# Kernel tuning notes

Hardware: AMD Instinct MI355X
Metric: run time of the kernel (lower is better)

The kernel has to match this reference:

```python
import jax, jax.numpy as jnp
import numpy as np
import math

B, S, E, H = 2, 2048, 1024, 16
D = E // H  # d_head = 64

def setup_inputs() -> dict:
    key = jax.random.key(0)
    ks = jax.random.split(key, 7)
    query = jax.random.normal(ks[0], (B, S, E), dtype=jnp.float32)
    k_in = jax.random.normal(ks[1], (B, S, E), dtype=jnp.float32)
    v_in = jax.random.normal(ks[2], (B, S, E), dtype=jnp.float32)
    # causal mask, broadcastable over batch and heads; mask==0 positions are blocked
    mask = jnp.tril(jnp.ones((S, S), dtype=jnp.int32))[None, None]
    scale = 1.0 / math.sqrt(E)
    w_q = jax.random.normal(ks[3], (E, E), dtype=jnp.float32) * scale
    w_k = jax.random.normal(ks[4], (E, E), dtype=jnp.float32) * scale
    w_v = jax.random.normal(ks[5], (E, E), dtype=jnp.float32) * scale
    w_o = jax.random.normal(ks[6], (E, E), dtype=jnp.float32) * scale
    return {"query": query, "key": k_in, "value": v_in, "mask": mask,
            "w_q": w_q, "w_k": w_k, "w_v": w_v, "w_o": w_o}

def reference(query, key, value, mask, w_q, w_k, w_v, w_o):
    # projections (nn.Linear with no bias: x @ W^T); split heads -> [B,H,S,D]
    q = (query @ w_q.T).reshape(B, S, H, D).transpose(0, 2, 1, 3)
    k = (key @ w_k.T).reshape(B, S, H, D).transpose(0, 2, 1, 3)
    v = (value @ w_v.T).reshape(B, S, H, D).transpose(0, 2, 1, 3)
    # scaled dot-product scores [B,H,S,S]
    scores = jnp.einsum('bhqd,bhkd->bhqk', q, k) / math.sqrt(D)
    scores = jnp.where(mask == 0, jnp.float32(-1e9), scores)
    attn = jax.nn.softmax(scores, axis=-1)  # dropout p=0.0 -> identity
    out = jnp.einsum('bhqk,bhkd->bhqd', attn, v)  # [B,H,S,D]
    out = out.transpose(0, 2, 1, 3).reshape(B, S, E)
    return out @ w_o.T
```

## Files before the change

### kernel.cpp

```cpp
#include <hip/hip_runtime.h>
#include <hip/hip_bf16.h>

#define B_ 2
#define S_ 2048
#define E_ 1024
#define H_ 16
#define D_ 64

typedef __attribute__((ext_vector_type(8))) short bf16x8;
typedef __attribute__((ext_vector_type(4))) float f32x4;

static __device__ __forceinline__ unsigned short f2bf(float x) {
    union { float f; unsigned u; } v; v.f = x;
    unsigned r = v.u + 0x7FFF + ((v.u >> 16) & 1);
    return (unsigned short)(r >> 16);
}

static __device__ __forceinline__ unsigned pack2bf(float a, float b) {
    union { float f; unsigned u; } x, y; x.f = a; y.f = b;
    unsigned ra = x.u + 0x7FFF + ((x.u >> 16) & 1);
    unsigned rb = y.u + 0x7FFF + ((y.u >> 16) & 1);
    return (ra >> 16) | (rb & 0xFFFF0000u);
}

static __device__ __forceinline__ unsigned packtrunc(float a, float b) {
    union { float f; unsigned u; } x, y; x.f = a; y.f = b;
    return __builtin_amdgcn_perm(y.u, x.u, 0x07060302);
}

static __device__ __forceinline__ void async_copy16(const void* gsrc, void* ldst) {
    __builtin_amdgcn_global_load_lds(
        (const __attribute__((address_space(1))) void*)gsrc,
        (__attribute__((address_space(3))) void*)ldst, 16, 0, 0);
}

__global__ void cvt_multi(const float* __restrict__ s0, const float* __restrict__ s1,
                          const float* __restrict__ s2, const float* __restrict__ s3,
                          unsigned short* __restrict__ dst, int n4,
                          float c0, float c1, float c2, float c3) {
    const float* src = (blockIdx.y == 0) ? s0 : (blockIdx.y == 1) ? s1
                     : (blockIdx.y == 2) ? s2 : s3;
    float c = (blockIdx.y == 0) ? c0 : (blockIdx.y == 1) ? c1
            : (blockIdx.y == 2) ? c2 : c3;
    int i = blockIdx.x * blockDim.x + threadIdx.x;
    if (i >= n4) return;
    float4 f = ((const float4*)src)[i];
    ushort4 o;
    o.x = f2bf(f.x * c); o.y = f2bf(f.y * c); o.z = f2bf(f.z * c); o.w = f2bf(f.w * c);
    ((ushort4*)(dst + (size_t)blockIdx.y * n4 * 4))[i] = o;
}

template <int MODE>
__global__ __launch_bounds__(256) void gemm128(
    const unsigned short* __restrict__ A0, const unsigned short* __restrict__ B0,
    void* __restrict__ C0, int M, int N, int K) {
    __shared__ __align__(16) unsigned short Al[128 * 64];
    __shared__ __align__(16) unsigned short Bl[128 * 64];
    const unsigned short* A = A0;
    const unsigned short* Bm = B0;
    int z = 0;
    if (MODE == 4) {
        z = blockIdx.z;
        A  = A0 + (size_t)z * 4194304;
        Bm = B0 + (size_t)z * 1048576;
    }
    const int bm = blockIdx.y * 128, bn = blockIdx.x * 128;
    const int tid = threadIdx.x;
    const int w = tid >> 6, lane = tid & 63;
    const int col = lane & 15, quad = lane >> 4, swz = col & 7;
    const int wm = (w >> 1) * 64, wn = (w & 1) * 64;

    f32x4 acc[4][4] = {};

    for (int k0 = 0; k0 < K; k0 += 64) {
        __syncthreads();
#pragma unroll
        for (int it = 0; it < 4; it++) {
            int s = tid + it * 256, r = s >> 3, cg = (s & 7) ^ (r & 7);
            async_copy16(A + (size_t)(bm + r) * K + k0 + cg * 8, &Al[s * 8]);
            async_copy16(Bm + (size_t)(bn + r) * K + k0 + cg * 8, &Bl[s * 8]);
        }
        __syncthreads();
#pragma unroll
        for (int h = 0; h < 2; h++) {
            const int cq = ((h * 4 + quad) ^ swz) * 8;
            bf16x8 af[4], bf[4];
#pragma unroll
            for (int i = 0; i < 4; i++) af[i] = *(const bf16x8*)&Al[(wm + i * 16 + col) * 64 + cq];
#pragma unroll
            for (int j = 0; j < 4; j++) bf[j] = *(const bf16x8*)&Bl[(wn + j * 16 + col) * 64 + cq];
#pragma unroll
            for (int i = 0; i < 4; i++)
#pragma unroll
                for (int j = 0; j < 4; j++)
                    acc[i][j] = __builtin_amdgcn_mfma_f32_16x16x32_bf16(af[i], bf[j], acc[i][j], 0, 0, 0);
        }
    }

    if (MODE == 3) {
#pragma unroll
        for (int i = 0; i < 4; i++)
#pragma unroll
            for (int j = 0; j < 4; j++)
#pragma unroll
                for (int r = 0; r < 4; r++) {
                    int gm = bm + wm + i * 16 + quad * 4 + r;
                    int gn = bn + wn + j * 16 + col;
                    ((float*)C0)[(size_t)gm * N + gn] = acc[i][j][r];
                }
    } else {
        __syncthreads();
        unsigned short* scr = ((w < 2) ? Al : Bl) + (w & 1) * 4096;
        const int b  = (bm + wm) >> 11;
        const int s0 = (bm + wm) & 2047;
        const int hh = (bn + wn) >> 6;
        unsigned short* outp = (unsigned short*)C0 + (size_t)z * 4194304;
        if (z == 2) {
#pragma unroll
            for (int i = 0; i < 4; i++)
#pragma unroll
                for (int j = 0; j < 4; j++) {
                    int n = j * 16 + col;
                    int c = i * 2 + (quad >> 1);
                    uint2 pk;
                    pk.x = pack2bf(acc[i][j][0], acc[i][j][1]);
                    pk.y = pack2bf(acc[i][j][2], acc[i][j][3]);
                    *(uint2*)&scr[n * 64 + ((c ^ (n & 7)) << 3) + ((quad & 1) << 2)] = pk;
                }
#pragma unroll
            for (int it = 0; it < 8; it++) {
                int slot = it * 64 + lane, n = slot >> 3, c = slot & 7;
                uint4 v = *(uint4*)&scr[n * 64 + ((c ^ (n & 7)) << 3)];
                *(uint4*)&outp[(((size_t)b * H_ + hh) * D_ + n) * S_ + s0 + c * 8] = v;
            }
        } else {
#pragma unroll
            for (int i = 0; i < 4; i++)
#pragma unroll
                for (int j = 0; j < 4; j++)
#pragma unroll
                    for (int r = 0; r < 4; r++) {
                        int m = i * 16 + quad * 4 + r, n = j * 16 + col;
                        scr[m * 64 + (((n >> 3) ^ (m & 7)) << 3) + (n & 7)] = f2bf(acc[i][j][r]);
                    }
#pragma unroll
            for (int it = 0; it < 8; it++) {
                int slot = it * 64 + lane, m = slot >> 3, c = slot & 7;
                uint4 v = *(uint4*)&scr[m * 64 + ((c ^ (m & 7)) << 3)];
                *(uint4*)&outp[(((size_t)b * H_ + hh) * S_ + s0 + m) * (size_t)D_ + c * 8] = v;
            }
        }
    }
}

__global__ __launch_bounds__(256) void attn_kernel(
    const unsigned short* __restrict__ Q, const unsigned short* __restrict__ K_,
    const unsigned short* __restrict__ Vt, unsigned short* __restrict__ Out) {
    __shared__ __align__(16) unsigned short Kl[2][64 * 64];
    __shared__ __align__(16) unsigned short Vl[2][64 * 64];
    const int bh = blockIdx.y;
    const int qb = (bh >= 16) ? (int)blockIdx.x : 15 - (int)blockIdx.x;
    const int q0 = qb * 128;
    const int tid = threadIdx.x;
    const int w = tid >> 6, lane = tid & 63;
    const int col = lane & 15, quad = lane >> 4, swz = col & 7;
    const int qw0 = q0 + w * 32;
    const float NINF = -__builtin_huge_valf();

    const unsigned short* Qh = Q + (size_t)bh * S_ * D_;
    const unsigned short* Kh = K_ + (size_t)bh * S_ * D_;
    const unsigned short* Vh = Vt + (size_t)bh * D_ * S_;

    bf16x8 qf[2][2];
#pragma unroll
    for (int i = 0; i < 2; i++)
#pragma unroll
        for (int h = 0; h < 2; h++)
            qf[i][h] = *(const bf16x8*)(Qh + (size_t)(qw0 + i * 16 + col) * 64 + h * 32 + quad * 8);

    f32x4 o[2][4] = {};
    float lsum[2] = {0.f, 0.f};

#pragma unroll
    for (int it = 0; it < 2; it++) {
        int s = tid + it * 256, r = s >> 3, cg = (s & 7) ^ (r & 7);
        async_copy16(Kh + (size_t)r * 64 + cg * 8, &Kl[0][s * 8]);
        async_copy16(Vh + (size_t)r * S_ + cg * 8, &Vl[0][s * 8]);
    }

    const int nk = 2 * (qb + 1);
    for (int kt = 0; kt < nk; kt++) {
        const int k0 = kt * 64;
        const int cur = kt & 1;
        __syncthreads();
        if (kt + 1 < nk) {
            const int k1 = k0 + 64, nb = cur ^ 1;
#pragma unroll
            for (int it = 0; it < 2; it++) {
                int s = tid + it * 256, r = s >> 3, cg = (s & 7) ^ (r & 7);
                async_copy16(Kh + (size_t)(k1 + r) * 64 + cg * 8, &Kl[nb][s * 8]);
                async_copy16(Vh + (size_t)r * S_ + k1 + cg * 8, &Vl[nb][s * 8]);
            }
        }
        if (k0 > qw0 + 31) continue;

        const unsigned short* Kb = &Kl[cur][0];
        const unsigned short* Vb = &Vl[cur][0];

        f32x4 sc[2][4] = {};
#pragma unroll
        for (int h = 0; h < 2; h++) {
            const int cq = ((h * 4 + quad) ^ swz) * 8;
#pragma unroll
            for (int ct = 0; ct < 4; ct++) {
                bf16x8 kf = *(const bf16x8*)&Kb[(ct * 16 + col) * 64 + cq];
                sc[0][ct] = __builtin_amdgcn_mfma_f32_16x16x32_bf16(kf, qf[0][h], sc[0][ct], 0, 0, 0);
                sc[1][ct] = __builtin_amdgcn_mfma_f32_16x16x32_bf16(kf, qf[1][h], sc[1][ct], 0, 0, 0);
            }
        }
        if (k0 + 63 <= qw0) {
#pragma unroll
            for (int i = 0; i < 2; i++)
#pragma unroll
                for (int ct = 0; ct < 4; ct++) {
#pragma unroll
                    for (int r = 0; r < 4; r++)
                        sc[i][ct][r] = __builtin_amdgcn_exp2f(sc[i][ct][r]);
                    lsum[i] += (sc[i][ct][0] + sc[i][ct][1]) + (sc[i][ct][2] + sc[i][ct][3]);
                }
        } else {
#pragma unroll
            for (int i = 0; i < 2; i++)
#pragma unroll
                for (int ct = 0; ct < 4; ct++) {
#pragma unroll
                    for (int r = 0; r < 4; r++) {
                        int key = k0 + ct * 16 + quad * 4 + r;
                        int qi = qw0 + i * 16 + col;
                        float s = (key <= qi) ? sc[i][ct][r] : NINF;
                        sc[i][ct][r] = __builtin_amdgcn_exp2f(s);
                    }
                    lsum[i] += (sc[i][ct][0] + sc[i][ct][1]) + (sc[i][ct][2] + sc[i][ct][3]);
                }
        }
        union { bf16x8 v; unsigned u[4]; } pf[2][2];
#pragma unroll
        for (int i = 0; i < 2; i++)
#pragma unroll
            for (int kh = 0; kh < 2; kh++) {
                pf[i][kh].u[0] = packtrunc(sc[i][2 * kh][0], sc[i][2 * kh][1]);
                pf[i][kh].u[1] = packtrunc(sc[i][2 * kh][2], sc[i][2 * kh][3]);
                pf[i][kh].u[2] = packtrunc(sc[i][2 * kh + 1][0], sc[i][2 * kh + 1][1]);
                pf[i][kh].u[3] = packtrunc(sc[i][2 * kh + 1][2], sc[i][2 * kh + 1][3]);
            }
#pragma unroll
        for (int kh = 0; kh < 2; kh++)
#pragma unroll
            for (int dt = 0; dt < 4; dt++) {
                const int row = dt * 16 + col;
                const int ko0 = kh * 32 + quad * 4;
                const int ko1 = ko0 + 16;
                union { bf16x8 v; uint2 d2[2]; } vf;
                vf.d2[0] = *(const uint2*)&Vb[row * 64 + (((ko0 >> 3) ^ (row & 7)) << 3) + (ko0 & 7)];
                vf.d2[1] = *(const uint2*)&Vb[row * 64 + (((ko1 >> 3) ^ (row & 7)) << 3) + (ko1 & 7)];
#pragma unroll
                for (int i = 0; i < 2; i++)
                    o[i][dt] = __builtin_amdgcn_mfma_f32_16x16x32_bf16(vf.v, pf[i][kh].v, o[i][dt], 0, 0, 0);
            }
    }

    const int b = bh >> 4, hh = bh & 15;
#pragma unroll
    for (int i = 0; i < 2; i++) {
        float l = lsum[i];
        l += __shfl_xor(l, 16);
        l += __shfl_xor(l, 32);
        float inv = 1.f / l;
        int gq = qw0 + i * 16 + col;
#pragma unroll
        for (int dt = 0; dt < 4; dt++) {
            uint2 pk;
            pk.x = pack2bf(o[i][dt][0] * inv, o[i][dt][1] * inv);
            pk.y = pack2bf(o[i][dt][2] * inv, o[i][dt][3] * inv);
            *(uint2*)&Out[((size_t)b * S_ + gq) * E_ + hh * 64 + dt * 16 + quad * 4] = pk;
        }
    }
}

extern "C" void kernel_launch(void* const* d_in, const int* in_sizes, int n_in,
                              void* d_out, int out_size, void* d_ws, size_t ws_size,
                              hipStream_t stream) {
    const float* query = (const float*)d_in[0];
    const float* key_i = (const float*)d_in[1];
    const float* value = (const float*)d_in[2];
    const float* w_q = (const float*)d_in[4];
    const float* w_k = (const float*)d_in[5];
    const float* w_v = (const float*)d_in[6];
    const float* w_o = (const float*)d_in[7];
    float* out = (float*)d_out;

    const int M = B_ * S_;
    const int N = E_, K = E_;
    const size_t nX = (size_t)M * E_;
    const size_t nW = (size_t)E_ * E_;

    char* ws = (char*)d_ws;
    unsigned short* xq  = (unsigned short*)(ws);
    unsigned short* wqb = (unsigned short*)(ws + (24u << 20));
    unsigned short* Qb  = (unsigned short*)(ws + (32u << 20));
    unsigned short* Kb  = (unsigned short*)(ws + (40u << 20));
    unsigned short* Vtb = (unsigned short*)(ws + (48u << 20));
    unsigned short* Ab  = (unsigned short*)(ws + (56u << 20));

    const float SCQ = 0.125f * 1.44269504088896f;

    int n4x = (int)(nX / 4), n4w = (int)(nW / 4);
    cvt_multi<<<dim3((n4x + 255) / 256, 3), 256, 0, stream>>>(
        query, key_i, value, value, xq, n4x, 1.f, 1.f, 1.f, 1.f);
    cvt_multi<<<dim3((n4w + 255) / 256, 4), 256, 0, stream>>>(
        w_q, w_k, w_v, w_o, wqb, n4w, SCQ, 1.f, 1.f, 1.f);

    gemm128<4><<<dim3(N / 128, M / 128, 3), 256, 0, stream>>>(xq, wqb, Qb, M, N, K);

    attn_kernel<<<dim3(S_ / 128, B_ * H_), 256, 0, stream>>>(Qb, Kb, Vtb, Ab);

    gemm128<3><<<dim3(N / 128, M / 128), 256, 0, stream>>>(
        Ab, wqb + 3u * 1048576u, out, M, N, K);
}
```

Before: 241.4 us.

## Double-buffer LDS tiles in bf16 GEMM to overlap loads with MFMA

The GEMM kernel now keeps two LDS buffers for the A and B tiles. It issues the async global-to-LDS copies for the next K tile before running the MFMAs on the current tile, with a prologue that loads the first tile. This removes one barrier per iteration and is meant to hide global memory latency behind compute. The cost is twice the LDS per block (64KB instead of 32KB), which can lower occupancy. Correctness relies on the barrier waiting for the outstanding async copies.

```diff
diff --git a/kernel.cpp b/kernel.cpp
--- a/kernel.cpp
+++ b/kernel.cpp
@@ -54,8 +54,8 @@
 __global__ __launch_bounds__(256) void gemm128(
     const unsigned short* __restrict__ A0, const unsigned short* __restrict__ B0,
     void* __restrict__ C0, int M, int N, int K) {
-    __shared__ __align__(16) unsigned short Al[128 * 64];
-    __shared__ __align__(16) unsigned short Bl[128 * 64];
+    __shared__ __align__(16) unsigned short Al[2][128 * 64];
+    __shared__ __align__(16) unsigned short Bl[2][128 * 64];
     const unsigned short* A = A0;
     const unsigned short* Bm = B0;
     int z = 0;
@@ -72,23 +72,36 @@
 
     f32x4 acc[4][4] = {};
 
-    for (int k0 = 0; k0 < K; k0 += 64) {
+#pragma unroll
+    for (int it = 0; it < 4; it++) {
+        int s = tid + it * 256, r = s >> 3, cg = (s & 7) ^ (r & 7);
+        async_copy16(A + (size_t)(bm + r) * K + cg * 8, &Al[0][s * 8]);
+        async_copy16(Bm + (size_t)(bn + r) * K + cg * 8, &Bl[0][s * 8]);
+    }
+
+    const int nk = K >> 6;
+    for (int kt = 0; kt < nk; kt++) {
+        const int cur = kt & 1;
         __syncthreads();
-#pragma unroll
-        for (int it = 0; it < 4; it++) {
-            int s = tid + it * 256, r = s >> 3, cg = (s & 7) ^ (r & 7);
-            async_copy16(A + (size_t)(bm + r) * K + k0 + cg * 8, &Al[s * 8]);
-            async_copy16(Bm + (size_t)(bn + r) * K + k0 + cg * 8, &Bl[s * 8]);
-        }
-        __syncthreads();
+        if (kt + 1 < nk) {
+            const int k1 = (kt + 1) << 6, nb = cur ^ 1;
+#pragma unroll
+            for (int it = 0; it < 4; it++) {
+                int s = tid + it * 256, r = s >> 3, cg = (s & 7) ^ (r & 7);
+                async_copy16(A + (size_t)(bm + r) * K + k1 + cg * 8, &Al[nb][s * 8]);
+                async_copy16(Bm + (size_t)(bn + r) * K + k1 + cg * 8, &Bl[nb][s * 8]);
+            }
+        }
+        const unsigned short* Ab = &Al[cur][0];
+        const unsigned short* Bb = &Bl[cur][0];
 #pragma unroll
         for (int h = 0; h < 2; h++) {
             const int cq = ((h * 4 + quad) ^ swz) * 8;
             bf16x8 af[4], bf[4];
 #pragma unroll
-            for (int i = 0; i < 4; i++) af[i] = *(const bf16x8*)&Al[(wm + i * 16 + col) * 64 + cq];
-#pragma unroll
-            for (int j = 0; j < 4; j++) bf[j] = *(const bf16x8*)&Bl[(wn + j * 16 + col) * 64 + cq];
+            for (int i = 0; i < 4; i++) af[i] = *(const bf16x8*)&Ab[(wm + i * 16 + col) * 64 + cq];
+#pragma unroll
+            for (int j = 0; j < 4; j++) bf[j] = *(const bf16x8*)&Bb[(wn + j * 16 + col) * 64 + cq];
 #pragma unroll
             for (int i = 0; i < 4; i++)
 #pragma unroll
@@ -110,7 +123,7 @@
                 }
     } else {
         __syncthreads();
-        unsigned short* scr = ((w < 2) ? Al : Bl) + (w & 1) * 4096;
+        unsigned short* scr = ((w < 2) ? &Al[0][0] : &Bl[0][0]) + (w & 1) * 4096;
         const int b  = (bm + wm) >> 11;
         const int s0 = (bm + wm) & 2047;
         const int hh = (bn + wn) >> 6;
```

Result: faster. 232.5 us (-3.7%).
